# Kernel optimization log

Hardware: AMD Instinct MI355X
Metric: run time of the kernel (lower is better)

The kernel has to match this reference:

```python
import jax, jax.numpy as jnp
import numpy as np

E_DIM = 64  # head dim, scale = 1/sqrt(E)

def setup_inputs() -> dict:
    key = jax.random.key(0)
    k1, k2, k3 = jax.random.split(key, 3)
    B, L, H, E = 4, 2048, 8, 64
    queries = jax.random.normal(k1, (B, L, H, E), dtype=jnp.float32)
    keys = jax.random.normal(k2, (B, L, H, E), dtype=jnp.float32)
    values = jax.random.normal(k3, (B, L, H, E), dtype=jnp.float32)
    return {"queries": queries, "keys": keys, "values": values}

def reference(queries, keys, values):
    # queries: [B,L,H,E], keys: [B,S,H,E], values: [B,S,H,D]; L == S
    E = queries.shape[-1]
    scale = 1.0 / jnp.sqrt(jnp.asarray(E, dtype=queries.dtype))
    scores = jnp.einsum('blhe,bshe->bhls', queries, keys)  # [B,H,L,S]
    series = jax.nn.softmax(scale * scores, axis=-1)       # dropout p=0.0 -> identity
    V = jnp.einsum('bhls,bshd->blhd', series, values)      # [B,L,H,D]
    return V
```

## Files before the change

### kernel.cpp

```cpp
#include <hip/hip_runtime.h>

typedef __attribute__((ext_vector_type(4)))  float    f32x4;
typedef __attribute__((ext_vector_type(16))) float    f32x16;
typedef __attribute__((ext_vector_type(8)))  _Float16 half8;
typedef __attribute__((ext_vector_type(2)))  __fp16   fp16x2;
typedef __attribute__((ext_vector_type(4)))  _Float16 half4;
typedef __attribute__((ext_vector_type(8)))  short    short8;

#define SCL2E 0.18033688011112042f

__device__ __forceinline__ unsigned short f2h_bits(float x) {
    union { _Float16 h; unsigned short u; } c;
    c.h = (_Float16)x;
    return c.u;
}

__device__ __forceinline__ void gl_lds16(const unsigned short* g, unsigned short* l) {
    __builtin_amdgcn_global_load_lds((const __attribute__((address_space(1))) void*)g,
                                     (__attribute__((address_space(3))) void*)l, 16, 0, 0);
}

__global__ __launch_bounds__(256)
void cvt_kv_kernel(const float* __restrict__ K, const float* __restrict__ V,
                   unsigned short* __restrict__ wsK, unsigned short* __restrict__ wsV) {
    int bid = blockIdx.x;
    if (bid < 4096) {
        int t   = bid * 256 + threadIdx.x;
        int eg  = t & 15;
        int gr  = t >> 4;
        int kv  = gr & 2047, bh = gr >> 11;
        int b = bh >> 3, h = bh & 7;
        const float* sp = K + (((size_t)b * 2048 + kv) * 8 + h) * 64 + eg * 4;
        f32x4 v = *(const f32x4*)sp;
        int T = kv >> 6, R = kv & 31, half = (kv >> 5) & 1;
        int egp = (eg & ~3) | ((eg & 1) << 1) | ((eg >> 1) & 1);
        int gnl = (half * 8 + (egp >> 1)) ^ (R & 15);
        size_t idx = (((size_t)bh * 32 + T) * 32 + R) * 128 + gnl * 8 + (egp & 1) * 4;
        union { unsigned short s[4]; unsigned long long u; } o;
        o.s[0] = f2h_bits(v[0]); o.s[1] = f2h_bits(v[1]);
        o.s[2] = f2h_bits(v[2]); o.s[3] = f2h_bits(v[3]);
        *(unsigned long long*)(wsK + idx) = o.u;
    } else {
        int t   = (bid - 4096) * 256 + threadIdx.x;
        int d   = t & 63;
        int g   = t >> 6;
        int kv4 = g & 511, bh = g >> 9;
        int b = bh >> 3, h = bh & 7;
        int kv = kv4 * 4;
        const float* sp = V + (((size_t)b * 2048 + kv) * 8 + h) * 64 + d;
        float v0 = sp[0], v1 = sp[512], v2 = sp[1024], v3 = sp[1536];
        int T = kv >> 6, R = d & 31, halfd = d >> 5;
        int kvg  = (kv >> 2) & 15;
        int kvgp = (kvg & ~3) | ((kvg & 1) << 1) | ((kvg >> 1) & 1);
        int gnl  = (halfd * 8 + (kvgp >> 1)) ^ (R & 15);
        size_t idx = (((size_t)bh * 32 + T) * 32 + R) * 128 + gnl * 8 + (kvgp & 1) * 4;
        union { unsigned short s[4]; unsigned long long u; } o;
        o.s[0] = f2h_bits(v0); o.s[1] = f2h_bits(v1);
        o.s[2] = f2h_bits(v2); o.s[3] = f2h_bits(v3);
        *(unsigned long long*)(wsV + idx) = o.u;
    }
}

__global__ __launch_bounds__(256, 4)
void attn_v8_kernel(const float* __restrict__ Q,
                    const unsigned short* __restrict__ wsK,
                    const unsigned short* __restrict__ wsV,
                    float* __restrict__ O) {
    __shared__ __align__(16) unsigned short lds[2][2][4096];

    const int tid  = threadIdx.x;
    const int lane = tid & 63;
    const int w    = tid >> 6;
    const int qw   = w & 1;
    const int kh   = w >> 1;
    const int lq   = lane & 31;
    const int hi   = lane >> 5;

    const int bid = blockIdx.x;
    const int xcd = bid & 7, slot = bid >> 3;
    const int qt  = slot & 31;
    const int bh  = ((slot >> 5) << 3) | xcd;
    const int q0  = qt * 64;
    const int b   = bh >> 3, h = bh & 7;

    const unsigned short* Ksrc = wsK + (size_t)bh * 32 * 4096;
    const unsigned short* Vsrc = wsV + (size_t)bh * 32 * 4096;
    float* Og = O + ((size_t)b * 2048 * 8 + (size_t)h) * 64;

    half8 qf[4];
    {
        const float* qp = Q + (((size_t)b * 2048 + q0 + qw * 32 + lq) * 8 + h) * 64;
#pragma unroll
        for (int ks = 0; ks < 4; ++ks) {
            f32x4 a = *(const f32x4*)(qp + 16 * ks + 4 * hi);
            f32x4 c = *(const f32x4*)(qp + 16 * ks + 8 + 4 * hi);
            union { fp16x2 h2[4]; half8 v; } u;
            u.h2[0] = __builtin_amdgcn_cvt_pkrtz(a[0] * SCL2E, a[1] * SCL2E);
            u.h2[1] = __builtin_amdgcn_cvt_pkrtz(a[2] * SCL2E, a[3] * SCL2E);
            u.h2[2] = __builtin_amdgcn_cvt_pkrtz(c[0] * SCL2E, c[1] * SCL2E);
            u.h2[3] = __builtin_amdgcn_cvt_pkrtz(c[2] * SCL2E, c[3] * SCL2E);
            qf[ks] = u.v;
        }
    }

#pragma unroll
    for (int p = 0; p < 2; ++p) {
        int c = tid + 256 * p;
        gl_lds16(Ksrc + c * 8, &lds[0][0][c * 8]);
        gl_lds16(Vsrc + c * 8, &lds[0][1][c * 8]);
    }
    __syncthreads();

    int ofk[4], ofv0[2], ofv1[2];
#pragma unroll
    for (int ks = 0; ks < 4; ++ks) ofk[ks] = (((kh * 8 + ks * 2 + hi) ^ (lq & 15)) << 3);
#pragma unroll
    for (int kc = 0; kc < 2; ++kc) {
        ofv0[kc] = (((kh * 4 + kc * 2 + hi)     ^ (lq & 15)) << 3);
        ofv1[kc] = (((8 + kh * 4 + kc * 2 + hi) ^ (lq & 15)) << 3);
    }

    f32x16 acc0 = {0.f,0.f,0.f,0.f,0.f,0.f,0.f,0.f,0.f,0.f,0.f,0.f,0.f,0.f,0.f,0.f};
    f32x16 acc1 = acc0;
    float lrow = 0.f;
    const fp16x2 vone = {(__fp16)1.0f, (__fp16)1.0f};

    for (int t = 0; t < 32; ++t) {
        const int cur = t & 1;
        if (t + 1 < 32) {
            const int nxt = cur ^ 1;
#pragma unroll
            for (int p = 0; p < 2; ++p) {
                int c = tid + 256 * p;
                gl_lds16(Ksrc + (size_t)(t + 1) * 4096 + c * 8, &lds[nxt][0][c * 8]);
                gl_lds16(Vsrc + (size_t)(t + 1) * 4096 + c * 8, &lds[nxt][1][c * 8]);
            }
        }

        const unsigned short* kb = &lds[cur][0][0];
        f32x16 s = {0.f,0.f,0.f,0.f,0.f,0.f,0.f,0.f,0.f,0.f,0.f,0.f,0.f,0.f,0.f,0.f};
        __builtin_amdgcn_s_setprio(1);
#pragma unroll
        for (int ks = 0; ks < 4; ++ks) {
            half8 kf = *(const half8*)&kb[lq * 128 + ofk[ks]];
            s = __builtin_amdgcn_mfma_f32_32x32x16_f16(kf, qf[ks], s, 0, 0, 0);
        }
        __builtin_amdgcn_s_setprio(0);

        half8 pf[2];
        float pA = 0.f, pB = 0.f;
#pragma unroll
        for (int kc = 0; kc < 2; ++kc) {
            union { fp16x2 h2[4]; half8 v; } u;
#pragma unroll
            for (int j = 0; j < 4; ++j) {
                float e0 = __builtin_amdgcn_exp2f(s[8 * kc + 2 * j]);
                float e1 = __builtin_amdgcn_exp2f(s[8 * kc + 2 * j + 1]);
                u.h2[j] = __builtin_amdgcn_cvt_pkrtz(e0, e1);
#if __has_builtin(__builtin_amdgcn_fdot2)
                if (kc == 0) pA = __builtin_amdgcn_fdot2(u.h2[j], vone, pA, false);
                else         pB = __builtin_amdgcn_fdot2(u.h2[j], vone, pB, false);
#else
                if (kc == 0) pA += e0 + e1; else pB += e0 + e1;
#endif
            }
            pf[kc] = u.v;
        }
        lrow += pA + pB;

        const unsigned short* vb = &lds[cur][1][0];
        __builtin_amdgcn_s_setprio(1);
#pragma unroll
        for (int kc = 0; kc < 2; ++kc) {
            half8 vf0 = *(const half8*)&vb[lq * 128 + ofv0[kc]];
            half8 vf1 = *(const half8*)&vb[lq * 128 + ofv1[kc]];
            acc0 = __builtin_amdgcn_mfma_f32_32x32x16_f16(vf0, pf[kc], acc0, 0, 0, 0);
            acc1 = __builtin_amdgcn_mfma_f32_32x32x16_f16(vf1, pf[kc], acc1, 0, 0, 0);
        }
        __builtin_amdgcn_s_setprio(0);

        __syncthreads();
    }

    lrow += __shfl_xor(lrow, 32);

    float* mlds = (float*)&lds[0][0][0];
    const int mslot = (qw * 64 + lane) * 36;
    if (kh) {
        float* dst = mlds + mslot;
#pragma unroll
        for (int a = 0; a < 4; ++a) {
            *(f32x4*)(dst + 4 * a)      = (f32x4){acc0[4*a], acc0[4*a+1], acc0[4*a+2], acc0[4*a+3]};
            *(f32x4*)(dst + 16 + 4 * a) = (f32x4){acc1[4*a], acc1[4*a+1], acc1[4*a+2], acc1[4*a+3]};
        }
        dst[32] = lrow;
    }
    __syncthreads();
    if (!kh) {
        const float* src = mlds + mslot;
        float inv = 1.0f / (lrow + src[32]);

        const int qg = q0 + qw * 32 + lq;
        float* orow = Og + (size_t)qg * 512;
#pragma unroll
        for (int a = 0; a < 4; ++a) {
            f32x4 p0 = *(const f32x4*)(src + 4 * a);
            f32x4 p1 = *(const f32x4*)(src + 16 + 4 * a);
            f32x4 o0, o1;
#pragma unroll
            for (int i = 0; i < 4; ++i) {
                o0[i] = (acc0[4 * a + i] + p0[i]) * inv;
                o1[i] = (acc1[4 * a + i] + p1[i]) * inv;
            }
            *(f32x4*)(orow + 8 * a + 4 * hi)      = o0;
            *(f32x4*)(orow + 32 + 8 * a + 4 * hi) = o1;
        }
    }
}

__device__ __forceinline__ unsigned short f2bf(float f) {
    union { float f; unsigned u; } v; v.f = f;
    unsigned u = v.u;
    u += 0x7fffu + ((u >> 16) & 1u);
    return (unsigned short)(u >> 16);
}

__global__ __launch_bounds__(128, 2)
void attn_v1_kernel(const float* __restrict__ Q, const float* __restrict__ K,
                    const float* __restrict__ V, float* __restrict__ O) {
    __shared__ __align__(16) unsigned short lds_q[64 * 64];
    __shared__ __align__(16) unsigned short lds_k[64 * 64];
    __shared__ __align__(16) unsigned short lds_v[64 * 64];

    const int tid = threadIdx.x, lane = tid & 63, wv = tid >> 6;
    const int lq = lane & 15, g = lane >> 4;
    const int bid = blockIdx.x, xcd = bid & 7, slot = bid >> 3;
    const int qt = slot & 31;
    const int bh = ((slot >> 5) << 3) | xcd;
    const int b = bh >> 3, h = bh & 7;
    const size_t base = ((size_t)b * 2048 * 8 + (size_t)h) * 64;
    const float* Qg = Q + base; const float* Kg = K + base;
    const float* Vg = V + base; float* Og = O + base;
    const int q0 = qt * 64;
    const float S2E = 0.125f * 1.44269504088896341f;

#pragma unroll
    for (int p = 0; p < 16; ++p) {
        int r = (tid >> 5) + p * 4, e = (tid & 31) * 2;
        const float* src = Qg + (size_t)(q0 + r) * 512 + e;
        unsigned pk = (unsigned)f2bf(src[0]) | ((unsigned)f2bf(src[1]) << 16);
        *(unsigned*)&lds_q[(r * 64 + e) ^ ((r & 7) << 3)] = pk;
    }
    __syncthreads();
    short8 qf[2][2];
#pragma unroll
    for (int qc = 0; qc < 2; ++qc) {
        int row = wv * 32 + qc * 16 + lq;
#pragma unroll
        for (int j = 0; j < 2; ++j)
            qf[qc][j] = *(const short8*)&lds_q[(row * 64 + j * 32 + g * 8) ^ ((row & 7) << 3)];
    }
    f32x4 acc[2][4];
#pragma unroll
    for (int qc = 0; qc < 2; ++qc)
#pragma unroll
        for (int dc = 0; dc < 4; ++dc) acc[qc][dc] = (f32x4){0.f, 0.f, 0.f, 0.f};
    float mrow[2] = {-1e30f, -1e30f}, lrow[2] = {0.f, 0.f};

    for (int t = 0; t < 32; ++t) {
        const int kv0 = t * 64;
        __syncthreads();
#pragma unroll
        for (int p = 0; p < 16; ++p) {
            int r = (tid >> 5) + p * 4, e = (tid & 31) * 2;
            const float* src = Kg + (size_t)(kv0 + r) * 512 + e;
            unsigned pk = (unsigned)f2bf(src[0]) | ((unsigned)f2bf(src[1]) << 16);
            *(unsigned*)&lds_k[(r * 64 + e) ^ ((r & 7) << 3)] = pk;
        }
#pragma unroll
        for (int p = 0; p < 16; ++p) {
            int d = tid & 63, kv = (p * 2 + (tid >> 6)) * 2;
            float v0 = Vg[(size_t)(kv0 + kv) * 512 + d];
            float v1 = Vg[(size_t)(kv0 + kv + 1) * 512 + d];
            union { _Float16 hh[2]; unsigned u; } pk;
            pk.hh[0] = (_Float16)v0; pk.hh[1] = (_Float16)v1;
            *(unsigned*)&lds_v[(d * 64 + kv) ^ ((d & 15) << 2)] = pk.u;
        }
        __syncthreads();
        f32x4 sfr[2][4];
#pragma unroll
        for (int kc = 0; kc < 4; ++kc) {
            int row = kc * 16 + lq;
            short8 kf0 = *(const short8*)&lds_k[(row * 64 + 0 + g * 8) ^ ((row & 7) << 3)];
            short8 kf1 = *(const short8*)&lds_k[(row * 64 + 32 + g * 8) ^ ((row & 7) << 3)];
#pragma unroll
            for (int qc = 0; qc < 2; ++qc) {
                f32x4 sx = __builtin_amdgcn_mfma_f32_16x16x32_bf16(kf0, qf[qc][0], (f32x4){0.f,0.f,0.f,0.f}, 0, 0, 0);
                sx = __builtin_amdgcn_mfma_f32_16x16x32_bf16(kf1, qf[qc][1], sx, 0, 0, 0);
                sfr[qc][kc] = sx;
            }
        }
        half4 pfv[2][4];
#pragma unroll
        for (int qc = 0; qc < 2; ++qc) {
            float smax = -1e30f;
#pragma unroll
            for (int kc = 0; kc < 4; ++kc)
#pragma unroll
                for (int r = 0; r < 4; ++r) smax = fmaxf(smax, sfr[qc][kc][r]);
            smax = fmaxf(smax, __shfl_xor(smax, 16));
            smax = fmaxf(smax, __shfl_xor(smax, 32));
            float mn = fmaxf(mrow[qc], smax);
            float alpha = __builtin_amdgcn_exp2f((mrow[qc] - mn) * S2E);
            mrow[qc] = mn;
            float msc = mn * S2E, psum = 0.f;
#pragma unroll
            for (int kc = 0; kc < 4; ++kc)
#pragma unroll
                for (int r = 0; r < 4; ++r) {
                    float p = __builtin_amdgcn_exp2f(sfr[qc][kc][r] * S2E - msc);
                    psum += p;
                    pfv[qc][kc][r] = (_Float16)p;
                }
            psum += __shfl_xor(psum, 16);
            psum += __shfl_xor(psum, 32);
            lrow[qc] = lrow[qc] * alpha + psum;
#pragma unroll
            for (int dc = 0; dc < 4; ++dc) acc[qc][dc] *= alpha;
        }
#pragma unroll
        for (int dc = 0; dc < 4; ++dc) {
            int dd = dc * 16 + lq;
#pragma unroll
            for (int kc = 0; kc < 4; ++kc) {
                half4 vf = *(const half4*)&lds_v[(dd * 64 + kc * 16 + g * 4) ^ ((dd & 15) << 2)];
                acc[0][dc] = __builtin_amdgcn_mfma_f32_16x16x16f16(vf, pfv[0][kc], acc[0][dc], 0, 0, 0);
                acc[1][dc] = __builtin_amdgcn_mfma_f32_16x16x16f16(vf, pfv[1][kc], acc[1][dc], 0, 0, 0);
            }
        }
    }
#pragma unroll
    for (int qc = 0; qc < 2; ++qc) {
        float inv = 1.f / lrow[qc];
        int qrow = q0 + wv * 32 + qc * 16 + lq;
#pragma unroll
        for (int dc = 0; dc < 4; ++dc) {
            f32x4 o = acc[qc][dc] * inv;
            *(f32x4*)(Og + (size_t)qrow * 512 + dc * 16 + g * 4) = o;
        }
    }
}

extern "C" void kernel_launch(void* const* d_in, const int* in_sizes, int n_in,
                              void* d_out, int out_size, void* d_ws, size_t ws_size,
                              hipStream_t stream) {
    const float* Q = (const float*)d_in[0];
    const float* K = (const float*)d_in[1];
    const float* V = (const float*)d_in[2];
    float* O = (float*)d_out;

    const size_t per = (size_t)32 * 2048 * 64;
    const size_t need = 2 * per * sizeof(unsigned short);
    if (ws_size >= need) {
        unsigned short* wsK = (unsigned short*)d_ws;
        unsigned short* wsV = wsK + per;
        cvt_kv_kernel<<<dim3(8192), dim3(256), 0, stream>>>(K, V, wsK, wsV);
        attn_v8_kernel<<<dim3(1024), dim3(256), 0, stream>>>(Q, wsK, wsV, O);
    } else {
        attn_v1_kernel<<<dim3(1024), dim3(128), 0, stream>>>(Q, K, V, O);
    }
}
```

Before: 63.74 us.

## Load K/V MFMA fragments directly from global in lane order, drop LDS staging

The conversion kernel now writes K and V in fp16 in the exact per-lane MFMA fragment order, so each wave can read its operands straight from global memory with coalesced 16-byte loads. The LDS double buffer, the async global-to-LDS copies and the per-iteration __syncthreads are removed, and LDS is kept only for the final cross-wave merge. This is meant to cut LDS traffic and barrier stalls, but the loads are no longer prefetched one tile ahead, so global/L2 latency may sit exposed in front of the MFMAs. Waves sharing a query tile also reread the same K/V tile from cache instead of sharing one LDS copy.

```diff
diff --git a/kernel.cpp b/kernel.cpp
--- a/kernel.cpp
+++ b/kernel.cpp
@@ -13,11 +13,6 @@
     union { _Float16 h; unsigned short u; } c;
     c.h = (_Float16)x;
     return c.u;
-}
-
-__device__ __forceinline__ void gl_lds16(const unsigned short* g, unsigned short* l) {
-    __builtin_amdgcn_global_load_lds((const __attribute__((address_space(1))) void*)g,
-                                     (__attribute__((address_space(3))) void*)l, 16, 0, 0);
 }
 
 __global__ __launch_bounds__(256)
@@ -32,10 +27,13 @@
         int b = bh >> 3, h = bh & 7;
         const float* sp = K + (((size_t)b * 2048 + kv) * 8 + h) * 64 + eg * 4;
         f32x4 v = *(const f32x4*)sp;
-        int T = kv >> 6, R = kv & 31, half = (kv >> 5) & 1;
-        int egp = (eg & ~3) | ((eg & 1) << 1) | ((eg >> 1) & 1);
-        int gnl = (half * 8 + (egp >> 1)) ^ (R & 15);
-        size_t idx = (((size_t)bh * 32 + T) * 32 + R) * 128 + gnl * 8 + (egp & 1) * 4;
+        int T    = kv >> 6;
+        int kh   = (kv >> 5) & 1;
+        int ks   = eg >> 2;
+        int hi   = eg & 1;
+        int lane = (kv & 31) + 32 * hi;
+        int joff = 4 * ((eg >> 1) & 1);
+        size_t idx = (((size_t)bh * 32 + T) * 4096) + ((kh * 4 + ks) * 64 + lane) * 8 + joff;
         union { unsigned short s[4]; unsigned long long u; } o;
         o.s[0] = f2h_bits(v[0]); o.s[1] = f2h_bits(v[1]);
         o.s[2] = f2h_bits(v[2]); o.s[3] = f2h_bits(v[3]);
@@ -49,11 +47,16 @@
         int kv = kv4 * 4;
         const float* sp = V + (((size_t)b * 2048 + kv) * 8 + h) * 64 + d;
         float v0 = sp[0], v1 = sp[512], v2 = sp[1024], v3 = sp[1536];
-        int T = kv >> 6, R = d & 31, halfd = d >> 5;
-        int kvg  = (kv >> 2) & 15;
-        int kvgp = (kvg & ~3) | ((kvg & 1) << 1) | ((kvg >> 1) & 1);
-        int gnl  = (halfd * 8 + (kvgp >> 1)) ^ (R & 15);
-        size_t idx = (((size_t)bh * 32 + T) * 32 + R) * 128 + gnl * 8 + (kvgp & 1) * 4;
+        int T    = kv >> 6;
+        int kvt  = kv & 63;
+        int kh   = kvt >> 5;
+        int kvh  = kvt & 31;
+        int kc   = kvh >> 4;
+        int hi   = (kvh >> 2) & 1;
+        int joff = 4 * ((kvh >> 3) & 1);
+        int dh   = d >> 5;
+        int lane = (d & 31) + 32 * hi;
+        size_t idx = (((size_t)bh * 32 + T) * 4096) + ((kh * 4 + dh * 2 + kc) * 64 + lane) * 8 + joff;
         union { unsigned short s[4]; unsigned long long u; } o;
         o.s[0] = f2h_bits(v0); o.s[1] = f2h_bits(v1);
         o.s[2] = f2h_bits(v2); o.s[3] = f2h_bits(v3);
@@ -62,11 +65,11 @@
 }
 
 __global__ __launch_bounds__(256, 4)
-void attn_v8_kernel(const float* __restrict__ Q,
+void attn_v9_kernel(const float* __restrict__ Q,
                     const unsigned short* __restrict__ wsK,
                     const unsigned short* __restrict__ wsV,
                     float* __restrict__ O) {
-    __shared__ __align__(16) unsigned short lds[2][2][4096];
+    __shared__ __align__(16) float mlds[4608];
 
     const int tid  = threadIdx.x;
     const int lane = tid & 63;
@@ -83,8 +86,8 @@
     const int q0  = qt * 64;
     const int b   = bh >> 3, h = bh & 7;
 
-    const unsigned short* Ksrc = wsK + (size_t)bh * 32 * 4096;
-    const unsigned short* Vsrc = wsV + (size_t)bh * 32 * 4096;
+    const unsigned short* Ksrc = wsK + (size_t)bh * 32 * 4096 + (kh * 4) * 512;
+    const unsigned short* Vsrc = wsV + (size_t)bh * 32 * 4096 + (kh * 4) * 512;
     float* Og = O + ((size_t)b * 2048 * 8 + (size_t)h) * 64;
 
     half8 qf[4];
@@ -103,48 +106,30 @@
         }
     }
 
-#pragma unroll
-    for (int p = 0; p < 2; ++p) {
-        int c = tid + 256 * p;
-        gl_lds16(Ksrc + c * 8, &lds[0][0][c * 8]);
-        gl_lds16(Vsrc + c * 8, &lds[0][1][c * 8]);
-    }
-    __syncthreads();
-
-    int ofk[4], ofv0[2], ofv1[2];
-#pragma unroll
-    for (int ks = 0; ks < 4; ++ks) ofk[ks] = (((kh * 8 + ks * 2 + hi) ^ (lq & 15)) << 3);
-#pragma unroll
-    for (int kc = 0; kc < 2; ++kc) {
-        ofv0[kc] = (((kh * 4 + kc * 2 + hi)     ^ (lq & 15)) << 3);
-        ofv1[kc] = (((8 + kh * 4 + kc * 2 + hi) ^ (lq & 15)) << 3);
-    }
-
     f32x16 acc0 = {0.f,0.f,0.f,0.f,0.f,0.f,0.f,0.f,0.f,0.f,0.f,0.f,0.f,0.f,0.f,0.f};
     f32x16 acc1 = acc0;
     float lrow = 0.f;
     const fp16x2 vone = {(__fp16)1.0f, (__fp16)1.0f};
 
     for (int t = 0; t < 32; ++t) {
-        const int cur = t & 1;
-        if (t + 1 < 32) {
-            const int nxt = cur ^ 1;
-#pragma unroll
-            for (int p = 0; p < 2; ++p) {
-                int c = tid + 256 * p;
-                gl_lds16(Ksrc + (size_t)(t + 1) * 4096 + c * 8, &lds[nxt][0][c * 8]);
-                gl_lds16(Vsrc + (size_t)(t + 1) * 4096 + c * 8, &lds[nxt][1][c * 8]);
-            }
-        }
-
-        const unsigned short* kb = &lds[cur][0][0];
+        const unsigned short* Kt = Ksrc + (size_t)t * 4096;
+        const unsigned short* Vt = Vsrc + (size_t)t * 4096;
+
+        half8 kf0 = *(const half8*)&Kt[(0 * 64 + lane) * 8];
+        half8 kf1 = *(const half8*)&Kt[(1 * 64 + lane) * 8];
+        half8 kf2 = *(const half8*)&Kt[(2 * 64 + lane) * 8];
+        half8 kf3 = *(const half8*)&Kt[(3 * 64 + lane) * 8];
+        half8 vf00 = *(const half8*)&Vt[(0 * 64 + lane) * 8];
+        half8 vf01 = *(const half8*)&Vt[(1 * 64 + lane) * 8];
+        half8 vf10 = *(const half8*)&Vt[(2 * 64 + lane) * 8];
+        half8 vf11 = *(const half8*)&Vt[(3 * 64 + lane) * 8];
+
         f32x16 s = {0.f,0.f,0.f,0.f,0.f,0.f,0.f,0.f,0.f,0.f,0.f,0.f,0.f,0.f,0.f,0.f};
         __builtin_amdgcn_s_setprio(1);
-#pragma unroll
-        for (int ks = 0; ks < 4; ++ks) {
-            half8 kf = *(const half8*)&kb[lq * 128 + ofk[ks]];
-            s = __builtin_amdgcn_mfma_f32_32x32x16_f16(kf, qf[ks], s, 0, 0, 0);
-        }
+        s = __builtin_amdgcn_mfma_f32_32x32x16_f16(kf0, qf[0], s, 0, 0, 0);
+        s = __builtin_amdgcn_mfma_f32_32x32x16_f16(kf1, qf[1], s, 0, 0, 0);
+        s = __builtin_amdgcn_mfma_f32_32x32x16_f16(kf2, qf[2], s, 0, 0, 0);
+        s = __builtin_amdgcn_mfma_f32_32x32x16_f16(kf3, qf[3], s, 0, 0, 0);
         __builtin_amdgcn_s_setprio(0);
 
         half8 pf[2];
@@ -168,23 +153,16 @@
         }
         lrow += pA + pB;
 
-        const unsigned short* vb = &lds[cur][1][0];
         __builtin_amdgcn_s_setprio(1);
-#pragma unroll
-        for (int kc = 0; kc < 2; ++kc) {
-            half8 vf0 = *(const half8*)&vb[lq * 128 + ofv0[kc]];
-            half8 vf1 = *(const half8*)&vb[lq * 128 + ofv1[kc]];
-            acc0 = __builtin_amdgcn_mfma_f32_32x32x16_f16(vf0, pf[kc], acc0, 0, 0, 0);
-            acc1 = __builtin_amdgcn_mfma_f32_32x32x16_f16(vf1, pf[kc], acc1, 0, 0, 0);
-        }
+        acc0 = __builtin_amdgcn_mfma_f32_32x32x16_f16(vf00, pf[0], acc0, 0, 0, 0);
+        acc1 = __builtin_amdgcn_mfma_f32_32x32x16_f16(vf10, pf[0], acc1, 0, 0, 0);
+        acc0 = __builtin_amdgcn_mfma_f32_32x32x16_f16(vf01, pf[1], acc0, 0, 0, 0);
+        acc1 = __builtin_amdgcn_mfma_f32_32x32x16_f16(vf11, pf[1], acc1, 0, 0, 0);
         __builtin_amdgcn_s_setprio(0);
-
-        __syncthreads();
     }
 
     lrow += __shfl_xor(lrow, 32);
 
-    float* mlds = (float*)&lds[0][0][0];
     const int mslot = (qw * 64 + lane) * 36;
     if (kh) {
         float* dst = mlds + mslot;
@@ -365,7 +343,7 @@
         unsigned short* wsK = (unsigned short*)d_ws;
         unsigned short* wsV = wsK + per;
         cvt_kv_kernel<<<dim3(8192), dim3(256), 0, stream>>>(K, V, wsK, wsV);
-        attn_v8_kernel<<<dim3(1024), dim3(256), 0, stream>>>(Q, wsK, wsV, O);
+        attn_v9_kernel<<<dim3(1024), dim3(256), 0, stream>>>(Q, wsK, wsV, O);
     } else {
         attn_v1_kernel<<<dim3(1024), dim3(128), 0, stream>>>(Q, K, V, O);
     }
```

After: 62.08 us. 2.6% less time.
